# Kernel tuning notes

Measured on AMD Instinct MI355X. Metric: run time of the kernel, lower is better.

## Reference

```python
import jax, jax.numpy as jnp
import numpy as np
from jax import lax

B, CIN, COUT, H, W, WDIM, K = 8, 256, 256, 64, 64, 512, 3
EPS = 1e-8
LRELU_SLOPE = 0.2


def setup_inputs() -> dict:
    key = jax.random.key(0)
    k_x, k_w, k_n, k_sw, k_cw = jax.random.split(key, 5)
    x = jax.random.normal(k_x, (B, CIN, H, W), dtype=jnp.float32)
    w = jax.random.normal(k_w, (B, WDIM), dtype=jnp.float32)
    noise = jax.random.normal(k_n, (B, 1, H, W), dtype=jnp.float32)
    # Equalized-LR params: stored ~N(0,1), scaled at use-time by 1/sqrt(fan_in)
    style_weight = jax.random.normal(k_sw, (CIN, WDIM), dtype=jnp.float32)
    style_bias = jnp.ones((CIN,), dtype=jnp.float32)  # StyleGAN style bias init = 1
    conv_weight = jax.random.normal(k_cw, (COUT, CIN, K, K), dtype=jnp.float32)
    noise_weight = jnp.zeros((COUT,), dtype=jnp.float32)  # NoiseInjection per-channel scale
    bias = jnp.zeros((COUT,), dtype=jnp.float32)
    return {"x": x, "w": w, "noise": noise, "style_weight": style_weight,
            "style_bias": style_bias, "conv_weight": conv_weight,
            "noise_weight": noise_weight, "bias": bias}


def reference(x, w, noise, style_weight, style_bias, conv_weight, noise_weight, bias):
    # EqualizedLinear: s = w @ (W * 1/sqrt(w_dim))^T + b  -> [B, CIN]
    s = jnp.einsum("bd,cd->bc", w, style_weight) * (1.0 / np.sqrt(WDIM)) + style_bias
    # Equalized conv weight scale
    wk = conv_weight * (1.0 / np.sqrt(CIN * K * K))  # [COUT, CIN, K, K]
    # Demodulation coefficient per (sample, out-channel):
    # demod = rsqrt(sum_{cin,kh,kw} (wk * s)^2 + eps)
    w2 = jnp.einsum("oikl,oikl->oi", wk, wk)               # [COUT, CIN]
    demod = lax.rsqrt(jnp.einsum("oi,bi->bo", w2, s * s) + EPS)  # [B, COUT]
    # Equivalent fused form: scale input per-channel, one shared conv, scale output
    xm = x * s[:, :, None, None]
    y = lax.conv_general_dilated(
        xm, wk, window_strides=(1, 1), padding="SAME",
        dimension_numbers=("NCHW", "OIHW", "NCHW"))
    y = y * demod[:, :, None, None]
    # NoiseInjection + bias + LeakyReLU(0.2)
    y = y + noise_weight[None, :, None, None] * noise + bias[None, :, None, None]
    return jnp.where(y >= 0, y, LRELU_SLOPE * y)
```

## Files before the change

### kernel.cpp

```cpp
#include <hip/hip_runtime.h>
#include <hip/hip_bf16.h>


typedef __attribute__((ext_vector_type(8))) short bf16x8;
typedef __attribute__((ext_vector_type(4))) float f32x4;

#define INV_SQRT_WDIM 0.04419417382415922f

__device__ __forceinline__ void gload_lds16(const void* g, void* l) {
  __builtin_amdgcn_global_load_lds(
      (const __attribute__((address_space(1))) void*)g,
      (__attribute__((address_space(3))) void*)l, 16, 0, 0);
}

__global__ __launch_bounds__(256)
void style2_kernel(const float* __restrict__ w, const float* __restrict__ sw,
                   const float* __restrict__ sb, float* __restrict__ s) {
  const int c = blockIdx.x, t = threadIdx.x;
  const int lane = t & 63, wvi = t >> 6;
  const float2 swv = *(const float2*)&sw[c * 512 + t * 2];
  __shared__ float red[4][8];
  float acc[8];
#pragma unroll
  for (int b = 0; b < 8; ++b) {
    const float2 wv2 = *(const float2*)&w[b * 512 + t * 2];
    acc[b] = swv.x * wv2.x + swv.y * wv2.y;
  }
#pragma unroll
  for (int b = 0; b < 8; ++b)
#pragma unroll
    for (int off = 32; off > 0; off >>= 1) acc[b] += __shfl_down(acc[b], off);
  if (lane == 0)
#pragma unroll
    for (int b = 0; b < 8; ++b) red[wvi][b] = acc[b];
  __syncthreads();
  if (t < 8) {
    float tot = red[0][t] + red[1][t] + red[2][t] + red[3][t];
    s[t * 256 + c] = tot * INV_SQRT_WDIM + sb[c];
  }
}

__global__ __launch_bounds__(256)
void wdm_kernel(const float* __restrict__ cw, const float* __restrict__ s,
                __hip_bfloat16* __restrict__ wt2, float* __restrict__ demod) {
  const int o = blockIdx.x, i = threadIdx.x;
  const int lane = i & 63, wvi = i >> 6;
  float v[9];
  float w2 = 0.f;
#pragma unroll
  for (int t = 0; t < 9; ++t) {
    v[t] = cw[(o * 256 + i) * 9 + t];
    w2 += v[t] * v[t];
  }
  const int wbase = (i >> 5) * 8192 + (o >> 4) * 512 + ((i >> 3) & 3) * 128 +
                    (o & 15) * 8 + (i & 7);
#pragma unroll
  for (int t = 0; t < 9; ++t)
    wt2[t * 65536 + wbase] = __float2bfloat16(v[t] * (1.0f / 48.0f));
  __shared__ float red[4][8];
  float pv[8];
#pragma unroll
  for (int b = 0; b < 8; ++b) {
    const float sv = s[b * 256 + i];
    pv[b] = w2 * sv * sv;
  }
#pragma unroll
  for (int b = 0; b < 8; ++b)
#pragma unroll
    for (int off = 32; off > 0; off >>= 1) pv[b] += __shfl_down(pv[b], off);
  if (lane == 0)
#pragma unroll
    for (int b = 0; b < 8; ++b) red[wvi][b] = pv[b];
  __syncthreads();
  if (i < 8) {
    float tot = red[0][i] + red[1][i] + red[2][i] + red[3][i];
    demod[i * 256 + o] = rsqrtf(tot * (1.0f / 2304.0f) + 1e-8f);
  }
}

__global__ __launch_bounds__(256)
void xmod_kernel(const float* __restrict__ x, const float* __restrict__ s,
                 __hip_bfloat16* __restrict__ xt) {
  const int h = blockIdx.x;
  const int b = blockIdx.y;
  __shared__ __hip_bfloat16 tile[256 * 66];
  const int t = threadIdx.x;
  const int wl4 = (t & 15) * 4;
#pragma unroll 4
  for (int p = 0; p < 16; ++p) {
    const int i = p * 16 + (t >> 4);
    const float4 v = *(const float4*)&x[((b * 256 + i) * 64 + h) * 64 + wl4];
    const float sv = s[b * 256 + i];
    const int wsw = wl4 ^ (((i >> 3) & 7) << 3);
    unsigned lo = ((unsigned)__bfloat16_as_ushort(__float2bfloat16(v.y * sv)) << 16) |
                  (unsigned)__bfloat16_as_ushort(__float2bfloat16(v.x * sv));
    unsigned hi = ((unsigned)__bfloat16_as_ushort(__float2bfloat16(v.w * sv)) << 16) |
                  (unsigned)__bfloat16_as_ushort(__float2bfloat16(v.z * sv));
    *(unsigned*)&tile[i * 66 + wsw] = lo;
    *(unsigned*)&tile[i * 66 + wsw + 2] = hi;
  }
  __syncthreads();
#pragma unroll 2
  for (int p = 0; p < 8; ++p) {
    const int w = p * 8 + (t >> 5);
    const int c = t & 31;
    ushort out8[8];
#pragma unroll
    for (int j = 0; j < 8; ++j) {
      const int i = c * 8 + j;
      const int wsw = w ^ (((i >> 3) & 7) << 3);
      out8[j] = __bfloat16_as_ushort(tile[i * 66 + wsw]);
    }
    const int slot = (c & 3) ^ ((w >> 1) & 3);
    *(uint4*)&xt[((b * 64 + h) * 64 + w) * 256 + (c >> 2) * 32 + slot * 8] =
        *(uint4*)out8;
  }
}

__global__ __launch_bounds__(256, 3)
void conv_mfma_kernel(const __hip_bfloat16* __restrict__ xt,
                      const __hip_bfloat16* __restrict__ wt2,
                      const float* __restrict__ demod,
                      const float* __restrict__ noise,
                      const float* __restrict__ nw,
                      const float* __restrict__ bias,
                      const __hip_bfloat16* __restrict__ zbuf,
                      float* __restrict__ out) {
  __shared__ __hip_bfloat16 xlds[2][12288] __attribute__((aligned(16)));

  const int tid = threadIdx.x;
  const int lane = tid & 63;
  const int wv = tid >> 6;

  const int h0 = blockIdx.x * 4;
  const int oc0 = blockIdx.y * 64;
  const int b = blockIdx.z;

  const int aoff = (lane >> 4) * 128 + (lane & 15) * 8;
  const int o16b = oc0 >> 4;

  int boff[4][3];
  bool bok[4][3];
#pragma unroll
  for (int q = 0; q < 4; ++q)
#pragma unroll
    for (int tj = 0; tj < 3; ++tj) {
      int wx = q * 16 + (lane & 15) + tj - 1;
      bool ok = (unsigned)wx < 64u;
      int wc = ok ? wx : 0;
      int slot = (lane >> 4) ^ ((wc >> 1) & 3);
      boff[q][tj] = wc * 32 + slot * 8;
      bok[q][tj] = ok;
    }

  const f32x4 zero4 = {0.f, 0.f, 0.f, 0.f};
  const bf16x8 zerov = {0, 0, 0, 0, 0, 0, 0, 0};
  f32x4 acc[4][4];
#pragma unroll
  for (int m = 0; m < 4; ++m)
#pragma unroll
    for (int q = 0; q < 4; ++q) acc[m][q] = zero4;

  auto stage = [&](int buf, int scc) {
#pragma unroll
    for (int k = 0; k < 6; ++k) {
      const int ch = wv * 6 + k;
      const int r = ch >> 2;
      const int wseg = ch & 3;
      const int gr = h0 - 1 + r;
      const __hip_bfloat16* src =
          ((unsigned)gr < 64u)
              ? xt + ((b * 64 + gr) * 64 + wseg * 16 + (lane >> 2)) * 256 +
                    scc * 32 + (lane & 3) * 8
              : zbuf;
      gload_lds16(src, &xlds[buf][ch * 512]);
    }
  };

  stage(0, 0);
  __syncthreads();

  for (int cc = 0; cc < 8; ++cc) {
    const int cur = cc & 1;
    if (cc < 7) stage(cur ^ 1, cc + 1);
#pragma unroll
    for (int ti = 0; ti < 3; ++ti) {
#pragma unroll
      for (int tj = 0; tj < 3; ++tj) {
        const int t = ti * 3 + tj;
        bf16x8 av[4];
#pragma unroll
        for (int m = 0; m < 4; ++m)
          av[m] = *(const bf16x8*)&wt2[t * 65536 + cc * 8192 +
                                       (o16b + m) * 512 + aoff];
#pragma unroll
        for (int q = 0; q < 4; ++q) {
          bf16x8 bv = *(const bf16x8*)&xlds[cur][(wv + ti) * 2048 + boff[q][tj]];
          if (!bok[q][tj]) bv = zerov;
#pragma unroll
          for (int m = 0; m < 4; ++m)
            acc[m][q] = __builtin_amdgcn_mfma_f32_16x16x32_bf16(av[m], bv,
                                                                acc[m][q], 0, 0, 0);
        }
      }
    }
    __syncthreads();
  }

  const int hrow = h0 + wv;
  float nzv[4];
#pragma unroll
  for (int q = 0; q < 4; ++q)
    nzv[q] = noise[b * 4096 + hrow * 64 + q * 16 + (lane & 15)];
#pragma unroll
  for (int m = 0; m < 4; ++m) {
#pragma unroll
    for (int reg = 0; reg < 4; ++reg) {
      const int oc = oc0 + m * 16 + (lane >> 4) * 4 + reg;
      const float dm = demod[b * 256 + oc];
      const float nwv = nw[oc];
      const float bvv = bias[oc];
#pragma unroll
      for (int q = 0; q < 4; ++q) {
        float v = acc[m][q][reg] * dm + nwv * nzv[q] + bvv;
        v = (v >= 0.f) ? v : 0.2f * v;
        out[((b * 256 + oc) * 64 + hrow) * 64 + q * 16 + (lane & 15)] = v;
      }
    }
  }
}

extern "C" void kernel_launch(void* const* d_in, const int* in_sizes, int n_in,
                              void* d_out, int out_size, void* d_ws, size_t ws_size,
                              hipStream_t stream) {
  const float* x     = (const float*)d_in[0];
  const float* w     = (const float*)d_in[1];
  const float* noise = (const float*)d_in[2];
  const float* sw    = (const float*)d_in[3];
  const float* sb    = (const float*)d_in[4];
  const float* cw    = (const float*)d_in[5];
  const float* nw    = (const float*)d_in[6];
  const float* bias  = (const float*)d_in[7];
  float* out = (float*)d_out;

  char* ws = (char*)d_ws;
  float* s            = (float*)(ws);
  float* demod        = (float*)(ws + 8192);
  __hip_bfloat16* zbuf = (__hip_bfloat16*)(ws + 16384);
  __hip_bfloat16* wt2 = (__hip_bfloat16*)(ws + 17408);
  __hip_bfloat16* xt  = (__hip_bfloat16*)(ws + 1197056);

  hipMemsetAsync(zbuf, 0, 1024, stream);
  style2_kernel<<<256, 256, 0, stream>>>(w, sw, sb, s);
  wdm_kernel<<<256, 256, 0, stream>>>(cw, s, wt2, demod);
  xmod_kernel<<<dim3(64, 8), 256, 0, stream>>>(x, s, xt);
  conv_mfma_kernel<<<dim3(16, 4, 8), 256, 0, stream>>>(
      xt, wt2, demod, noise, nw, bias, zbuf, out);
}
```

Measured before the change: 154.0 us.

## Stage conv weights in LDS and enlarge conv block to eight rows

The conv kernel now uses 512-thread blocks covering 8 output rows, so the grid halves. Each block stages the per-chunk weight slice into dynamic LDS together with the input halo, double-buffered, and the MFMA A-operands are read from LDS instead of global memory. The zero buffer memset is folded into the style kernel, which removes one launch. In exchange the kernel uses about 152KB of LDS per block, so only one block fits per CU, which limits occupancy and latency hiding.

Result: faster. 134.9 us (-12.4%).

```diff
diff --git a/kernel.cpp b/kernel.cpp
--- a/kernel.cpp
+++ b/kernel.cpp
@@ -15,9 +15,11 @@
 
 __global__ __launch_bounds__(256)
 void style2_kernel(const float* __restrict__ w, const float* __restrict__ sw,
-                   const float* __restrict__ sb, float* __restrict__ s) {
+                   const float* __restrict__ sb, float* __restrict__ s,
+                   unsigned* __restrict__ zbuf) {
   const int c = blockIdx.x, t = threadIdx.x;
   const int lane = t & 63, wvi = t >> 6;
+  if (c == 0) zbuf[t] = 0u;
   const float2 swv = *(const float2*)&sw[c * 512 + t * 2];
   __shared__ float red[4][8];
   float acc[8];
@@ -117,7 +119,7 @@
   }
 }
 
-__global__ __launch_bounds__(256, 3)
+__global__ __launch_bounds__(512, 2)
 void conv_mfma_kernel(const __hip_bfloat16* __restrict__ xt,
                       const __hip_bfloat16* __restrict__ wt2,
                       const float* __restrict__ demod,
@@ -126,18 +128,17 @@
                       const float* __restrict__ bias,
                       const __hip_bfloat16* __restrict__ zbuf,
                       float* __restrict__ out) {
-  __shared__ __hip_bfloat16 xlds[2][12288] __attribute__((aligned(16)));
+  extern __shared__ __hip_bfloat16 smem[];
 
   const int tid = threadIdx.x;
   const int lane = tid & 63;
   const int wv = tid >> 6;
 
-  const int h0 = blockIdx.x * 4;
+  const int h0 = blockIdx.x * 8;
   const int oc0 = blockIdx.y * 64;
   const int b = blockIdx.z;
 
   const int aoff = (lane >> 4) * 128 + (lane & 15) * 8;
-  const int o16b = oc0 >> 4;
 
   int boff[4][3];
   bool bok[4][3];
@@ -161,10 +162,10 @@
 #pragma unroll
     for (int q = 0; q < 4; ++q) acc[m][q] = zero4;
 
-  auto stage = [&](int buf, int scc) {
-#pragma unroll
-    for (int k = 0; k < 6; ++k) {
-      const int ch = wv * 6 + k;
+  auto stage = [&](__hip_bfloat16* buf, int scc) {
+#pragma unroll
+    for (int k = 0; k < 5; ++k) {
+      const int ch = wv * 5 + k;
       const int r = ch >> 2;
       const int wseg = ch & 3;
       const int gr = h0 - 1 + r;
@@ -173,16 +174,27 @@
               ? xt + ((b * 64 + gr) * 64 + wseg * 16 + (lane >> 2)) * 256 +
                     scc * 32 + (lane & 3) * 8
               : zbuf;
-      gload_lds16(src, &xlds[buf][ch * 512]);
+      gload_lds16(src, buf + ch * 512);
+    }
+#pragma unroll
+    for (int k = 0; k < 5; ++k) {
+      const int j = wv + 8 * k;
+      if (j < 36) {
+        const __hip_bfloat16* src = wt2 + (j >> 2) * 65536 + scc * 8192 +
+                                    (oc0 >> 4) * 512 + (j & 3) * 512 + lane * 8;
+        gload_lds16(src, buf + 20480 + j * 512);
+      }
     }
   };
 
-  stage(0, 0);
+  stage(smem, 0);
   __syncthreads();
 
   for (int cc = 0; cc < 8; ++cc) {
-    const int cur = cc & 1;
-    if (cc < 7) stage(cur ^ 1, cc + 1);
+    __hip_bfloat16* cbuf = smem + (cc & 1) * 38912;
+    __hip_bfloat16* nbuf = smem + ((cc & 1) ^ 1) * 38912;
+    if (cc < 7) stage(nbuf, cc + 1);
+    const __hip_bfloat16* wb = cbuf + 20480;
 #pragma unroll
     for (int ti = 0; ti < 3; ++ti) {
 #pragma unroll
@@ -191,11 +203,10 @@
         bf16x8 av[4];
 #pragma unroll
         for (int m = 0; m < 4; ++m)
-          av[m] = *(const bf16x8*)&wt2[t * 65536 + cc * 8192 +
-                                       (o16b + m) * 512 + aoff];
+          av[m] = *(const bf16x8*)&wb[t * 2048 + m * 512 + aoff];
 #pragma unroll
         for (int q = 0; q < 4; ++q) {
-          bf16x8 bv = *(const bf16x8*)&xlds[cur][(wv + ti) * 2048 + boff[q][tj]];
+          bf16x8 bv = *(const bf16x8*)&cbuf[(wv + ti) * 2048 + boff[q][tj]];
           if (!bok[q][tj]) bv = zerov;
 #pragma unroll
           for (int m = 0; m < 4; ++m)
@@ -246,14 +257,16 @@
   char* ws = (char*)d_ws;
   float* s            = (float*)(ws);
   float* demod        = (float*)(ws + 8192);
-  __hip_bfloat16* zbuf = (__hip_bfloat16*)(ws + 16384);
+  unsigned* zbuf      = (unsigned*)(ws + 16384);
   __hip_bfloat16* wt2 = (__hip_bfloat16*)(ws + 17408);
   __hip_bfloat16* xt  = (__hip_bfloat16*)(ws + 1197056);
 
-  hipMemsetAsync(zbuf, 0, 1024, stream);
-  style2_kernel<<<256, 256, 0, stream>>>(w, sw, sb, s);
+  hipFuncSetAttribute((const void*)conv_mfma_kernel,
+                      hipFuncAttributeMaxDynamicSharedMemorySize, 155648);
+
+  style2_kernel<<<256, 256, 0, stream>>>(w, sw, sb, s, zbuf);
   wdm_kernel<<<256, 256, 0, stream>>>(cw, s, wt2, demod);
   xmod_kernel<<<dim3(64, 8), 256, 0, stream>>>(x, s, xt);
-  conv_mfma_kernel<<<dim3(16, 4, 8), 256, 0, stream>>>(
-      xt, wt2, demod, noise, nw, bias, zbuf, out);
-}
+  conv_mfma_kernel<<<dim3(8, 4, 8), 512, 155648, stream>>>(
+      xt, wt2, demod, noise, nw, bias, (const __hip_bfloat16*)zbuf, out);
+}
```
